# Performance work log

Hardware: AMD Instinct MI355X
Metric: run time of the kernel (lower is better)

Reference implementation:

```python
import jax, jax.numpy as jnp
import numpy as np

RATIO = 0.2
MIX_ALPHA = 0.5
TEMPERATURE = 0.1
EPS = 1e-12  # F.normalize eps


def setup_inputs() -> dict:
    key = jax.random.key(0)
    z = jax.random.normal(key, (16384, 256), dtype=jnp.float32)
    return {"z": z}


def reference(z):
    B = z.shape[0]
    n_hard = max(1, int(B * RATIO))

    # L2-normalize rows (F.normalize with eps clamp)
    norm = jnp.maximum(jnp.linalg.norm(z, axis=-1, keepdims=True), EPS)
    z_norm = z / norm

    # [B, B] cosine similarity, diagonal excluded
    sim = z_norm @ z_norm.T
    diag = jnp.eye(B, dtype=bool)
    sim = jnp.where(diag, -jnp.inf, sim)
    logits = sim / TEMPERATURE  # softmax(logits) == sim_probs

    # Batched sampling: replaces the per-sample Python loop with one fused pass
    key = jax.random.key(42)
    k_src, k_tgt, k_alpha = jax.random.split(key, 3)
    src_idx = jax.random.randint(k_src, (n_hard,), 0, B)  # torch.randint
    # categorical over logits rows == multinomial over softmax probs
    tgt_idx = jax.random.categorical(k_tgt, logits[src_idx], axis=-1)
    alpha = jax.random.uniform(k_alpha, (n_hard, 1), dtype=z.dtype) * MIX_ALPHA

    hard_negs = alpha * z[src_idx] + (1.0 - alpha) * z[tgt_idx]  # [n_hard, D]
    return hard_negs
```

## Files before the change

### kernel.cpp

```cpp
#include <hip/hip_runtime.h>
#include <stdint.h>
#include <math.h>

#define BN 16384
#define DK 256
#define NH 3276
#define NJB 26
#define NCB 128

typedef __attribute__((ext_vector_type(8))) short short8;
typedef __attribute__((ext_vector_type(4))) short short4v;
typedef __attribute__((ext_vector_type(4))) float f32x4;

__host__ __device__ __forceinline__ uint32_t rotl32(uint32_t x, int d) {
#ifdef __HIP_DEVICE_COMPILE__
  return __builtin_amdgcn_alignbit(x, x, 32 - d);
#else
  return (x << d) | (x >> (32 - d));
#endif
}

__host__ __device__ __forceinline__ void tf2x32(uint32_t k0, uint32_t k1,
                                                uint32_t c0, uint32_t c1,
                                                uint32_t& o0, uint32_t& o1) {
  uint32_t ks2 = 0x1BD11BDAu ^ k0 ^ k1;
  uint32_t x0 = c0 + k0, x1 = c1 + k1;
#define RR(d) { x0 += x1; x1 = rotl32(x1, d); x1 ^= x0; }
  RR(13) RR(15) RR(26) RR(6)   x0 += k1;  x1 += ks2 + 1u;
  RR(17) RR(29) RR(16) RR(24)  x0 += ks2; x1 += k0  + 2u;
  RR(13) RR(15) RR(26) RR(6)   x0 += k0;  x1 += k1  + 3u;
  RR(17) RR(29) RR(16) RR(24)  x0 += k1;  x1 += ks2 + 4u;
  RR(13) RR(15) RR(26) RR(6)   x0 += ks2; x1 += k0  + 5u;
#undef RR
  o0 = x0; o1 = x1;
}

__device__ __forceinline__ uint32_t rand32_at(uint32_t k0, uint32_t k1, uint32_t p) {
  uint32_t x0, x1; tf2x32(k0, k1, 0u, p, x0, x1);
  return x0 ^ x1;
}

__device__ __forceinline__ float unif01_from_bits(uint32_t bits) {
  return __uint_as_float((bits >> 9) | 0x3f800000u) - 1.0f;
}

__device__ __forceinline__ float gumbel_at(uint32_t k0, uint32_t k1, uint32_t p) {
  uint32_t bits = rand32_at(k0, k1, p);
  float f = unif01_from_bits(bits);
  float u = fmaxf(f, 1.17549435e-38f);
  float t = __log2f(u) * (-0.69314718055994531f);
  return __log2f(t) * (-0.69314718055994531f);
}

__device__ __forceinline__ unsigned long long packvc(float v, uint32_t c) {
  uint32_t u = __float_as_uint(v);
  u ^= ((int32_t)u < 0) ? 0xFFFFFFFFu : 0x80000000u;
  return ((unsigned long long)u << 32) | (unsigned long long)(~c);
}

__device__ __forceinline__ void glds16(const unsigned short* g, short* l) {
  __builtin_amdgcn_global_load_lds(
      (const __attribute__((address_space(1))) void*)g,
      (__attribute__((address_space(3))) void*)l, 16, 0, 0);
}

__global__ __launch_bounds__(256) void k_prep(const float* __restrict__ z,
                                              unsigned short* __restrict__ zh,
                                              unsigned short* __restrict__ zl,
                                              int* __restrict__ src_idx,
                                              unsigned long long* __restrict__ best,
                                              uint32_t k20, uint32_t k21) {
  int b = blockIdx.x, t = threadIdx.x;
  if (b < BN / 4) {
    int row = b * 4 + (t >> 6), lane = t & 63;
    float4 v = *(const float4*)&z[row * DK + lane * 4];
    float ss = v.x * v.x + v.y * v.y + v.z * v.z + v.w * v.w;
#pragma unroll
    for (int off = 32; off; off >>= 1) ss += __shfl_xor(ss, off, 64);
    float inv = 1.0f / fmaxf(sqrtf(ss), 1e-12f);
    float f[4] = {v.x * inv, v.y * inv, v.z * inv, v.w * inv};
    short4v h, l;
#pragma unroll
    for (int i = 0; i < 4; ++i) {
      uint32_t u = __float_as_uint(f[i]);
      h[i] = (short)(u >> 16);
      float r = f[i] - __uint_as_float(u & 0xFFFF0000u);
      l[i] = (short)(__float_as_uint(r) >> 16);
    }
    *(short4v*)&zh[row * DK + lane * 4] = h;
    *(short4v*)&zl[row * DK + lane * 4] = l;
  } else {
    int i = (b - BN / 4) * 256 + t;
    if (i < NH) {
      uint32_t bits = rand32_at(k20, k21, (uint32_t)i);
      src_idx[i] = (int)(bits & (uint32_t)(BN - 1));
      best[i] = 0ull;
    }
  }
}

__global__ __launch_bounds__(256, 3) void k_main(const unsigned short* __restrict__ zh,
                                                 const unsigned short* __restrict__ zl,
                                                 const int* __restrict__ src_idx,
                                                 unsigned long long* __restrict__ best,
                                                 uint32_t kt0, uint32_t kt1) {
  __shared__ __align__(16) short As_hi[128 * 32];
  __shared__ __align__(16) short As_lo[128 * 32];
  __shared__ __align__(16) short Bs_hi[128 * 32];
  __shared__ __align__(16) short Bs_lo[128 * 32];

  const int flat = blockIdx.x;
  const int xcd = flat & 7, slot = flat >> 3;
  const int c_base = (xcd * 16 + (slot & 15)) * 128;
  const int j_base = (slot >> 4) * 128;

  const int t = threadIdx.x;
  const int lane = t & 63, w = t >> 6;

  const int r0 = w * 32 + (lane >> 2);
  const int r1 = r0 + 16;
  const int u0 = (lane & 3) ^ ((r0 >> 1) & 3);
  const int u1 = (lane & 3) ^ ((r1 >> 1) & 3);
  const int ga0 = src_idx[min(j_base + r0, NH - 1)];
  const int ga1 = src_idx[min(j_base + r1, NH - 1)];
  const uint32_t offA0 = (uint32_t)(ga0 * DK + u0 * 8);
  const uint32_t offA1 = (uint32_t)(ga1 * DK + u1 * 8);
  const uint32_t offB0 = (uint32_t)((c_base + r0) * DK + u0 * 8);
  const uint32_t offB1 = (uint32_t)((c_base + r1) * DK + u1 * 8);
  short* dA  = &As_hi[w * 1024];
  short* dAl = &As_lo[w * 1024];
  short* dB  = &Bs_hi[w * 1024];
  short* dBl = &Bs_lo[w * 1024];

  const int cl = lane & 15, q = lane >> 4;
  const int mb = (w >> 1) * 64 + cl;
  const int nb = (w & 1) * 64 + cl;

  f32x4 acc[4][4];
#pragma unroll
  for (int mt = 0; mt < 4; ++mt)
#pragma unroll
    for (int nt = 0; nt < 4; ++nt) acc[mt][nt] = (f32x4){0.f, 0.f, 0.f, 0.f};

#pragma unroll
  for (int kc = 0; kc < 8; ++kc) {
    const int ko = kc * 32;
    glds16(zh + offA0 + ko, dA);
    glds16(zh + offA1 + ko, dA + 512);
    glds16(zl + offA0 + ko, dAl);
    glds16(zl + offA1 + ko, dAl + 512);
    glds16(zh + offB0 + ko, dB);
    glds16(zh + offB1 + ko, dB + 512);
    glds16(zl + offB0 + ko, dBl);
    glds16(zl + offB1 + ko, dBl + 512);
    __syncthreads();

    short8 bh[4], bl[4];
#pragma unroll
    for (int nt = 0; nt < 4; ++nt) {
      int row = nb + nt * 16;
      int off = row * 32 + (q ^ ((row >> 1) & 3)) * 8;
      bh[nt] = *(const short8*)&Bs_hi[off];
      bl[nt] = *(const short8*)&Bs_lo[off];
    }
#pragma unroll
    for (int mt = 0; mt < 4; ++mt) {
      int row = mb + mt * 16;
      int off = row * 32 + (q ^ ((row >> 1) & 3)) * 8;
      short8 ah = *(const short8*)&As_hi[off];
      short8 al = *(const short8*)&As_lo[off];
#pragma unroll
      for (int nt = 0; nt < 4; ++nt) {
        acc[mt][nt] = __builtin_amdgcn_mfma_f32_16x16x32_bf16(ah, bh[nt], acc[mt][nt], 0, 0, 0);
        acc[mt][nt] = __builtin_amdgcn_mfma_f32_16x16x32_bf16(ah, bl[nt], acc[mt][nt], 0, 0, 0);
        acc[mt][nt] = __builtin_amdgcn_mfma_f32_16x16x32_bf16(al, bh[nt], acc[mt][nt], 0, 0, 0);
      }
    }
    __syncthreads();
  }

  const int q4 = (lane >> 4) * 4;
  const int coff = c_base + (w & 1) * 64;
  const int roff = j_base + (w >> 1) * 64;
  const uint32_t ccl = (uint32_t)(coff + cl);
#pragma unroll
  for (int mt = 0; mt < 4; ++mt)
#pragma unroll
    for (int r = 0; r < 4; ++r) {
      int gj = roff + mt * 16 + q4 + r;
      int s = src_idx[min(gj, NH - 1)];
      uint32_t pbase = (uint32_t)gj * (uint32_t)BN + ccl;
      float bv = -INFINITY; uint32_t bc = 0;
#pragma unroll
      for (int nt = 0; nt < 4; ++nt) {
        uint32_t c = ccl + (uint32_t)(nt * 16);
        float gv = gumbel_at(kt0, kt1, pbase + (uint32_t)(nt * 16));
        float tot = fmaf(acc[mt][nt][r], 10.0f, gv);
        tot = ((int)c == s) ? -INFINITY : tot;
        if (tot > bv) { bv = tot; bc = c; }
      }
      unsigned long long key = packvc(bv, bc);
#pragma unroll
      for (int off = 1; off <= 8; off <<= 1) {
        unsigned long long o = __shfl_xor(key, off, 64);
        if (o > key) key = o;
      }
      if (cl == 0 && gj < NH) atomicMax(&best[gj], key);
    }
}

__global__ __launch_bounds__(64) void k_out(const float* __restrict__ z,
                                            const int* __restrict__ src_idx,
                                            const unsigned long long* __restrict__ best,
                                            float* __restrict__ out,
                                            uint32_t ka0, uint32_t ka1) {
  int j = blockIdx.x;
  int lane = threadIdx.x;
  int s = src_idx[j];
  int tgt = (int)(~((uint32_t)(best[j] & 0xFFFFFFFFull)));
  uint32_t bits = rand32_at(ka0, ka1, (uint32_t)j);
  float alpha = unif01_from_bits(bits) * 0.5f;
  float om = 1.0f - alpha;
  float4 a = *(const float4*)&z[s * DK + lane * 4];
  float4 b = *(const float4*)&z[tgt * DK + lane * 4];
  float4 o;
  o.x = alpha * a.x + om * b.x;
  o.y = alpha * a.y + om * b.y;
  o.z = alpha * a.z + om * b.z;
  o.w = alpha * a.w + om * b.w;
  *(float4*)&out[j * DK + lane * 4] = o;
}

extern "C" void kernel_launch(void* const* d_in, const int* in_sizes, int n_in,
                              void* d_out, int out_size, void* d_ws, size_t ws_size,
                              hipStream_t stream) {
  const float* z = (const float*)d_in[0];
  float* out = (float*)d_out;
  char* ws = (char*)d_ws;
  int*                src_idx = (int*)(ws);
  unsigned long long* best    = (unsigned long long*)(ws + 16384);
  unsigned short*     zh      = (unsigned short*)(ws + 65536);
  unsigned short*     zl      = (unsigned short*)(ws + 65536 + 8388608);

  uint32_t r0 = 0u, r1 = 42u;
  uint32_t ks0, ks1, kt0, kt1, ka0, ka1, k20, k21;
  tf2x32(r0, r1, 0u, 0u, ks0, ks1);
  tf2x32(r0, r1, 0u, 1u, kt0, kt1);
  tf2x32(r0, r1, 0u, 2u, ka0, ka1);
  tf2x32(ks0, ks1, 0u, 1u, k20, k21);

  k_prep<<<dim3(BN / 4 + (NH + 255) / 256), dim3(256), 0, stream>>>(
      z, zh, zl, src_idx, best, k20, k21);
  k_main<<<dim3(NCB * NJB), dim3(256), 0, stream>>>(zh, zl, src_idx, best, kt0, kt1);
  k_out <<<dim3(NH), dim3(64), 0, stream>>>(z, src_idx, best, out, ka0, ka1);
}
```

Measured before the change: 263.9 us.

## Make main GEMM kernel persistent with double-buffered LDS prefetch

Replaces the 3328-block grid with 512 persistent blocks, each looping over 6–7 row tiles for a fixed column tile. Shared memory is double-buffered so the next k-chunk (and the first chunk of the next tile) is loaded while MFMAs run on the current one, removing one barrier per chunk. Occupancy hint drops from 3 to 2 blocks per CU to fit the doubled LDS. The rotate helper is also replaced by plain shifts, and with only 512 blocks the work may be spread unevenly, since 6 and 7 tiles per block differ.

```diff
diff --git a/kernel.cpp b/kernel.cpp
--- a/kernel.cpp
+++ b/kernel.cpp
@@ -5,27 +5,19 @@
 #define BN 16384
 #define DK 256
 #define NH 3276
-#define NJB 26
-#define NCB 128
+#define NTILE 3328
+#define NBLK 512
 
 typedef __attribute__((ext_vector_type(8))) short short8;
 typedef __attribute__((ext_vector_type(4))) short short4v;
 typedef __attribute__((ext_vector_type(4))) float f32x4;
-
-__host__ __device__ __forceinline__ uint32_t rotl32(uint32_t x, int d) {
-#ifdef __HIP_DEVICE_COMPILE__
-  return __builtin_amdgcn_alignbit(x, x, 32 - d);
-#else
-  return (x << d) | (x >> (32 - d));
-#endif
-}
 
 __host__ __device__ __forceinline__ void tf2x32(uint32_t k0, uint32_t k1,
                                                 uint32_t c0, uint32_t c1,
                                                 uint32_t& o0, uint32_t& o1) {
   uint32_t ks2 = 0x1BD11BDAu ^ k0 ^ k1;
   uint32_t x0 = c0 + k0, x1 = c1 + k1;
-#define RR(d) { x0 += x1; x1 = rotl32(x1, d); x1 ^= x0; }
+#define RR(d) { x0 += x1; x1 = (x1 << d) | (x1 >> (32 - d)); x1 ^= x0; }
   RR(13) RR(15) RR(26) RR(6)   x0 += k1;  x1 += ks2 + 1u;
   RR(17) RR(29) RR(16) RR(24)  x0 += ks2; x1 += k0  + 2u;
   RR(13) RR(15) RR(26) RR(6)   x0 += k0;  x1 += k1  + 3u;
@@ -99,20 +91,22 @@
   }
 }
 
-__global__ __launch_bounds__(256, 3) void k_main(const unsigned short* __restrict__ zh,
+__global__ __launch_bounds__(256, 2) void k_main(const unsigned short* __restrict__ zh,
                                                  const unsigned short* __restrict__ zl,
                                                  const int* __restrict__ src_idx,
                                                  unsigned long long* __restrict__ best,
                                                  uint32_t kt0, uint32_t kt1) {
-  __shared__ __align__(16) short As_hi[128 * 32];
-  __shared__ __align__(16) short As_lo[128 * 32];
-  __shared__ __align__(16) short Bs_hi[128 * 32];
-  __shared__ __align__(16) short Bs_lo[128 * 32];
-
-  const int flat = blockIdx.x;
-  const int xcd = flat & 7, slot = flat >> 3;
-  const int c_base = (xcd * 16 + (slot & 15)) * 128;
-  const int j_base = (slot >> 4) * 128;
+  __shared__ __align__(16) short As_hi[2 * 4096];
+  __shared__ __align__(16) short As_lo[2 * 4096];
+  __shared__ __align__(16) short Bs_hi[2 * 4096];
+  __shared__ __align__(16) short Bs_lo[2 * 4096];
+
+  const int b = blockIdx.x;
+  const int xcd = b & 7;
+  const int cslot = (b >> 3) & 15;
+  const int c_base = (xcd * 16 + cslot) * 128;
+  const int j0 = b >> 7;
+  const int ntiles = (b < 256) ? 7 : 6;
 
   const int t = threadIdx.x;
   const int lane = t & 63, w = t >> 6;
@@ -121,92 +115,124 @@
   const int r1 = r0 + 16;
   const int u0 = (lane & 3) ^ ((r0 >> 1) & 3);
   const int u1 = (lane & 3) ^ ((r1 >> 1) & 3);
-  const int ga0 = src_idx[min(j_base + r0, NH - 1)];
-  const int ga1 = src_idx[min(j_base + r1, NH - 1)];
-  const uint32_t offA0 = (uint32_t)(ga0 * DK + u0 * 8);
-  const uint32_t offA1 = (uint32_t)(ga1 * DK + u1 * 8);
   const uint32_t offB0 = (uint32_t)((c_base + r0) * DK + u0 * 8);
   const uint32_t offB1 = (uint32_t)((c_base + r1) * DK + u1 * 8);
-  short* dA  = &As_hi[w * 1024];
-  short* dAl = &As_lo[w * 1024];
-  short* dB  = &Bs_hi[w * 1024];
-  short* dBl = &Bs_lo[w * 1024];
 
   const int cl = lane & 15, q = lane >> 4;
   const int mb = (w >> 1) * 64 + cl;
   const int nb = (w & 1) * 64 + cl;
-
-  f32x4 acc[4][4];
-#pragma unroll
-  for (int mt = 0; mt < 4; ++mt)
-#pragma unroll
-    for (int nt = 0; nt < 4; ++nt) acc[mt][nt] = (f32x4){0.f, 0.f, 0.f, 0.f};
-
-#pragma unroll
-  for (int kc = 0; kc < 8; ++kc) {
-    const int ko = kc * 32;
-    glds16(zh + offA0 + ko, dA);
-    glds16(zh + offA1 + ko, dA + 512);
-    glds16(zl + offA0 + ko, dAl);
-    glds16(zl + offA1 + ko, dAl + 512);
-    glds16(zh + offB0 + ko, dB);
-    glds16(zh + offB1 + ko, dB + 512);
-    glds16(zl + offB0 + ko, dBl);
-    glds16(zl + offB1 + ko, dBl + 512);
-    __syncthreads();
-
-    short8 bh[4], bl[4];
-#pragma unroll
-    for (int nt = 0; nt < 4; ++nt) {
-      int row = nb + nt * 16;
-      int off = row * 32 + (q ^ ((row >> 1) & 3)) * 8;
-      bh[nt] = *(const short8*)&Bs_hi[off];
-      bl[nt] = *(const short8*)&Bs_lo[off];
-    }
-#pragma unroll
-    for (int mt = 0; mt < 4; ++mt) {
-      int row = mb + mt * 16;
-      int off = row * 32 + (q ^ ((row >> 1) & 3)) * 8;
-      short8 ah = *(const short8*)&As_hi[off];
-      short8 al = *(const short8*)&As_lo[off];
+  int foffA[4], foffB[4];
+#pragma unroll
+  for (int i = 0; i < 4; ++i) {
+    int ra = mb + i * 16, rb = nb + i * 16;
+    foffA[i] = ra * 32 + (q ^ ((ra >> 1) & 3)) * 8;
+    foffB[i] = rb * 32 + (q ^ ((rb >> 1) & 3)) * 8;
+  }
+  const int ldsw = w * 1024;
+
+  uint32_t offA0 = (uint32_t)(src_idx[min(j0 * 128 + r0, NH - 1)] * DK + u0 * 8);
+  uint32_t offA1 = (uint32_t)(src_idx[min(j0 * 128 + r1, NH - 1)] * DK + u1 * 8);
+
+  glds16(zh + offA0, &As_hi[ldsw]);
+  glds16(zh + offA1, &As_hi[ldsw + 512]);
+  glds16(zl + offA0, &As_lo[ldsw]);
+  glds16(zl + offA1, &As_lo[ldsw + 512]);
+  glds16(zh + offB0, &Bs_hi[ldsw]);
+  glds16(zh + offB1, &Bs_hi[ldsw + 512]);
+  glds16(zl + offB0, &Bs_lo[ldsw]);
+  glds16(zl + offB1, &Bs_lo[ldsw + 512]);
+
+  for (int it = 0; it < ntiles; ++it) {
+    const int j_base = (j0 + 4 * it) * 128;
+    uint32_t nA0 = 0, nA1 = 0;
+    const bool have_next = (it + 1 < ntiles);
+    if (have_next) {
+      int njb = (j0 + 4 * (it + 1)) * 128;
+      nA0 = (uint32_t)(src_idx[min(njb + r0, NH - 1)] * DK + u0 * 8);
+      nA1 = (uint32_t)(src_idx[min(njb + r1, NH - 1)] * DK + u1 * 8);
+    }
+
+    f32x4 acc[4][4];
+#pragma unroll
+    for (int mt = 0; mt < 4; ++mt)
+#pragma unroll
+      for (int nt = 0; nt < 4; ++nt) acc[mt][nt] = (f32x4){0.f, 0.f, 0.f, 0.f};
+
+#pragma unroll
+    for (int kc = 0; kc < 8; ++kc) {
+      const int pc = (kc & 1) * 4096;
+      const int pn = ((kc + 1) & 1) * 4096;
+      __syncthreads();
+      if (kc < 7) {
+        const int ko = (kc + 1) * 32;
+        glds16(zh + offA0 + ko, &As_hi[pn + ldsw]);
+        glds16(zh + offA1 + ko, &As_hi[pn + ldsw + 512]);
+        glds16(zl + offA0 + ko, &As_lo[pn + ldsw]);
+        glds16(zl + offA1 + ko, &As_lo[pn + ldsw + 512]);
+        glds16(zh + offB0 + ko, &Bs_hi[pn + ldsw]);
+        glds16(zh + offB1 + ko, &Bs_hi[pn + ldsw + 512]);
+        glds16(zl + offB0 + ko, &Bs_lo[pn + ldsw]);
+        glds16(zl + offB1 + ko, &Bs_lo[pn + ldsw + 512]);
+      } else if (have_next) {
+        glds16(zh + nA0, &As_hi[ldsw]);
+        glds16(zh + nA1, &As_hi[ldsw + 512]);
+        glds16(zl + nA0, &As_lo[ldsw]);
+        glds16(zl + nA1, &As_lo[ldsw + 512]);
+        glds16(zh + offB0, &Bs_hi[ldsw]);
+        glds16(zh + offB1, &Bs_hi[ldsw + 512]);
+        glds16(zl + offB0, &Bs_lo[ldsw]);
+        glds16(zl + offB1, &Bs_lo[ldsw + 512]);
+      }
+
+      short8 bh[4], bl[4];
 #pragma unroll
       for (int nt = 0; nt < 4; ++nt) {
-        acc[mt][nt] = __builtin_amdgcn_mfma_f32_16x16x32_bf16(ah, bh[nt], acc[mt][nt], 0, 0, 0);
-        acc[mt][nt] = __builtin_amdgcn_mfma_f32_16x16x32_bf16(ah, bl[nt], acc[mt][nt], 0, 0, 0);
-        acc[mt][nt] = __builtin_amdgcn_mfma_f32_16x16x32_bf16(al, bh[nt], acc[mt][nt], 0, 0, 0);
-      }
-    }
-    __syncthreads();
+        bh[nt] = *(const short8*)&Bs_hi[pc + foffB[nt]];
+        bl[nt] = *(const short8*)&Bs_lo[pc + foffB[nt]];
+      }
+#pragma unroll
+      for (int mt = 0; mt < 4; ++mt) {
+        short8 ah = *(const short8*)&As_hi[pc + foffA[mt]];
+        short8 al = *(const short8*)&As_lo[pc + foffA[mt]];
+#pragma unroll
+        for (int nt = 0; nt < 4; ++nt) {
+          acc[mt][nt] = __builtin_amdgcn_mfma_f32_16x16x32_bf16(ah, bh[nt], acc[mt][nt], 0, 0, 0);
+          acc[mt][nt] = __builtin_amdgcn_mfma_f32_16x16x32_bf16(ah, bl[nt], acc[mt][nt], 0, 0, 0);
+          acc[mt][nt] = __builtin_amdgcn_mfma_f32_16x16x32_bf16(al, bh[nt], acc[mt][nt], 0, 0, 0);
+        }
+      }
+    }
+    offA0 = nA0; offA1 = nA1;
+
+    const int q4 = (lane >> 4) * 4;
+    const int coff = c_base + (w & 1) * 64;
+    const int roff = j_base + (w >> 1) * 64;
+    const uint32_t ccl = (uint32_t)(coff + cl);
+#pragma unroll
+    for (int mt = 0; mt < 4; ++mt)
+#pragma unroll
+      for (int r = 0; r < 4; ++r) {
+        int gj = roff + mt * 16 + q4 + r;
+        int s = src_idx[min(gj, NH - 1)];
+        uint32_t pbase = (uint32_t)gj * (uint32_t)BN + ccl;
+        float bv = -INFINITY; uint32_t bc = 0;
+#pragma unroll
+        for (int nt = 0; nt < 4; ++nt) {
+          uint32_t c = ccl + (uint32_t)(nt * 16);
+          float gv = gumbel_at(kt0, kt1, pbase + (uint32_t)(nt * 16));
+          float tot = fmaf(acc[mt][nt][r], 10.0f, gv);
+          tot = ((int)c == s) ? -INFINITY : tot;
+          if (tot > bv) { bv = tot; bc = c; }
+        }
+        unsigned long long key = packvc(bv, bc);
+#pragma unroll
+        for (int off = 1; off <= 8; off <<= 1) {
+          unsigned long long o = __shfl_xor(key, off, 64);
+          if (o > key) key = o;
+        }
+        if (cl == 0 && gj < NH) atomicMax(&best[gj], key);
+      }
   }
-
-  const int q4 = (lane >> 4) * 4;
-  const int coff = c_base + (w & 1) * 64;
-  const int roff = j_base + (w >> 1) * 64;
-  const uint32_t ccl = (uint32_t)(coff + cl);
-#pragma unroll
-  for (int mt = 0; mt < 4; ++mt)
-#pragma unroll
-    for (int r = 0; r < 4; ++r) {
-      int gj = roff + mt * 16 + q4 + r;
-      int s = src_idx[min(gj, NH - 1)];
-      uint32_t pbase = (uint32_t)gj * (uint32_t)BN + ccl;
-      float bv = -INFINITY; uint32_t bc = 0;
-#pragma unroll
-      for (int nt = 0; nt < 4; ++nt) {
-        uint32_t c = ccl + (uint32_t)(nt * 16);
-        float gv = gumbel_at(kt0, kt1, pbase + (uint32_t)(nt * 16));
-        float tot = fmaf(acc[mt][nt][r], 10.0f, gv);
-        tot = ((int)c == s) ? -INFINITY : tot;
-        if (tot > bv) { bv = tot; bc = c; }
-      }
-      unsigned long long key = packvc(bv, bc);
-#pragma unroll
-      for (int off = 1; off <= 8; off <<= 1) {
-        unsigned long long o = __shfl_xor(key, off, 64);
-        if (o > key) key = o;
-      }
-      if (cl == 0 && gj < NH) atomicMax(&best[gj], key);
-    }
 }
 
 __global__ __launch_bounds__(64) void k_out(const float* __restrict__ z,
@@ -251,6 +277,6 @@
 
   k_prep<<<dim3(BN / 4 + (NH + 255) / 256), dim3(256), 0, stream>>>(
       z, zh, zl, src_idx, best, k20, k21);
-  k_main<<<dim3(NCB * NJB), dim3(256), 0, stream>>>(zh, zl, src_idx, best, kt0, kt1);
+  k_main<<<dim3(NBLK), dim3(256), 0, stream>>>(zh, zl, src_idx, best, kt0, kt1);
   k_out <<<dim3(NH), dim3(64), 0, stream>>>(z, src_idx, best, out, ka0, ka1);
 }
```

Measured after the change: 287.9 us. +9.1%, slower.
